# Performance work log

Measured on AMD Instinct MI355X. Metric: run time of the kernel, lower is better.

The kernel has to match this reference:

```python
import jax, jax.numpy as jnp
import numpy as np

B, S, H = 2, 2048, 2048
NH, NKV, HD = 16, 4, 128
ROPE_BASE = 10000.0


def setup_inputs() -> dict:
    key = jax.random.key(0)
    ks = jax.random.split(key, 5)
    x = jax.random.normal(ks[0], (B, S, H), dtype=jnp.float32)
    position_ids = jnp.arange(S, dtype=jnp.int64 if jax.config.jax_enable_x64 else jnp.int32).reshape(1, S)
    # Linear weights stored as [in, out] (equivalent to torch weight.T)
    sc = 1.0 / np.sqrt(H)
    Wq = jax.random.normal(ks[1], (H, NH * HD), dtype=jnp.float32) * sc
    Wk = jax.random.normal(ks[2], (H, NKV * HD), dtype=jnp.float32) * sc
    Wv = jax.random.normal(ks[3], (H, NKV * HD), dtype=jnp.float32) * sc
    Wo = jax.random.normal(ks[4], (NH * HD, H), dtype=jnp.float32) * (1.0 / np.sqrt(NH * HD))
    return {"x": x, "position_ids": position_ids, "Wq": Wq, "Wk": Wk, "Wv": Wv, "Wo": Wo}


def _rope(q, k, position_ids):
    # q: [B,S,NH,HD], k: [B,S,NKV,HD]; Llama-style half-split RoPE
    half = HD // 2
    inv_freq = 1.0 / (ROPE_BASE ** (jnp.arange(0, half, dtype=jnp.float32) * 2.0 / HD))
    ang = position_ids.astype(jnp.float32)[..., None] * inv_freq  # [b,S,half]
    cos = jnp.concatenate([jnp.cos(ang), jnp.cos(ang)], axis=-1)[:, :, None, :]  # [b,S,1,HD]
    sin = jnp.concatenate([jnp.sin(ang), jnp.sin(ang)], axis=-1)[:, :, None, :]

    def rot_half(t):
        t1, t2 = t[..., :half], t[..., half:]
        return jnp.concatenate([-t2, t1], axis=-1)

    return q * cos + rot_half(q) * sin, k * cos + rot_half(k) * sin


def reference(x, position_ids, Wq, Wk, Wv, Wo):
    b, s, _ = x.shape
    q = (x @ Wq).reshape(b, s, NH, HD)
    k = (x @ Wk).reshape(b, s, NKV, HD)
    v = (x @ Wv).reshape(b, s, NKV, HD)
    q, k = _rope(q, k, position_ids)
    reps = NH // NKV
    k = jnp.repeat(k, reps, axis=2)  # repeat_interleave on head dim
    v = jnp.repeat(v, reps, axis=2)
    q = q.transpose(0, 2, 1, 3)  # [b,h,s,d]
    k = k.transpose(0, 2, 1, 3)
    v = v.transpose(0, 2, 1, 3)
    scores = jnp.einsum('bhqd,bhkd->bhqk', q, k) / jnp.sqrt(jnp.float32(HD))
    causal = jnp.triu(jnp.ones((s, s), dtype=bool), k=1)
    scores = jnp.where(causal, -jnp.inf, scores)
    attn = jax.nn.softmax(scores.astype(jnp.float32), axis=-1).astype(q.dtype)
    out = jnp.einsum('bhqk,bhkd->bhqd', attn, v)
    out = out.transpose(0, 2, 1, 3).reshape(b, s, NH * HD)
    return out @ Wo
```

## Files before the change

### kernel.cpp

```cpp
#include <hip/hip_runtime.h>
#include <stdint.h>

typedef unsigned short u16;
typedef __attribute__((ext_vector_type(8))) short short8;
typedef __attribute__((ext_vector_type(4))) float floatx4;

#define S_LEN 2048
#define NQKV 3072

#if __has_builtin(__builtin_amdgcn_exp2f)
#define EXP2F __builtin_amdgcn_exp2f
#else
#define EXP2F exp2f
#endif

__device__ inline float bf2f(u16 u) {
  union { uint32_t u; float f; } v; v.u = ((uint32_t)u) << 16; return v.f;
}
__device__ inline u16 f2bf(float f) {
  union { float f; uint32_t u; } v; v.f = f;
  uint32_t r = v.u + 0x7fffu + ((v.u >> 16) & 1u);
  return (u16)(r >> 16);
}
__device__ inline void gl2lds16(const u16* g, u16* l) {
  __builtin_amdgcn_global_load_lds((const __attribute__((address_space(1))) uint32_t*)g,
                                   (__attribute__((address_space(3))) uint32_t*)l, 16, 0, 0);
}

__global__ void cast_k(const float* __restrict__ in, u16* __restrict__ out, int n4) {
  int i = blockIdx.x * 256 + threadIdx.x;
  if (i >= n4) return;
  float4 v = ((const float4*)in)[i];
  ushort4 o;
  o.x = f2bf(v.x); o.y = f2bf(v.y); o.z = f2bf(v.z); o.w = f2bf(v.w);
  ((ushort4*)out)[i] = o;
}

__global__ void transpose_k(const float* __restrict__ in, u16* __restrict__ out, int K, int N) {
  __shared__ u16 tile[32][33];
  int n0 = blockIdx.x * 32, k0 = blockIdx.y * 32;
  int tx = threadIdx.x, ty = threadIdx.y;
#pragma unroll
  for (int i = 0; i < 4; i++)
    tile[ty + 8 * i][tx] = f2bf(in[(size_t)(k0 + ty + 8 * i) * N + n0 + tx]);
  __syncthreads();
#pragma unroll
  for (int i = 0; i < 4; i++)
    out[(size_t)(n0 + ty + 8 * i) * K + k0 + tx] = tile[tx][ty + 8 * i];
}

__global__ void vtrans_k(const u16* __restrict__ qkv, u16* __restrict__ vt) {
  __shared__ u16 tile[32][33];
  int bk = blockIdx.x * 32, bd = blockIdx.y * 32, bz = blockIdx.z;
  int bb = bz >> 2, kvh = bz & 3;
  const u16* src = qkv + ((size_t)bb * S_LEN) * NQKV + 2560 + kvh * 128;
  u16* dst = vt + (size_t)bz * 128 * 2048;
  int tx = threadIdx.x, ty = threadIdx.y;
#pragma unroll
  for (int i = 0; i < 4; i++)
    tile[ty + 8 * i][tx] = src[(size_t)(bk + ty + 8 * i) * NQKV + bd + tx];
  __syncthreads();
#pragma unroll
  for (int i = 0; i < 4; i++)
    dst[(size_t)(bd + ty + 8 * i) * 2048 + bk + tx] = tile[tx][ty + 8 * i];
}

template <bool OUTF32>
__global__ __launch_bounds__(256) void gemm_bt(const u16* __restrict__ A, const u16* __restrict__ Bt,
                                               void* __restrict__ Cv, int M, int N, int K) {
  __shared__ u16 As[128 * 32];
  __shared__ u16 Bs[128 * 32];
  const int m0 = blockIdx.y * 128, n0 = blockIdx.x * 128;
  const int t = threadIdx.x, w = t >> 6, lane = t & 63;
  const int quad = lane >> 4, l16 = lane & 15;
  const int wm = (w >> 1) * 64, wn = (w & 1) * 64;
  const int lrow = lane >> 2, lk = (lane & 3) * 8;
  floatx4 acc[4][4] = {};
  for (int k0 = 0; k0 < K; k0 += 32) {
#pragma unroll
    for (int c = 2 * w; c <= 2 * w + 1; ++c) {
      int row = c * 16 + lrow;
      gl2lds16(A + (size_t)(m0 + row) * K + k0 + lk, As + c * 512 + lane * 8);
      gl2lds16(Bt + (size_t)(n0 + row) * K + k0 + lk, Bs + c * 512 + lane * 8);
    }
    __syncthreads();
    short8 a[4], b[4];
#pragma unroll
    for (int mt = 0; mt < 4; mt++) a[mt] = *(const short8*)(As + (wm + mt * 16 + l16) * 32 + quad * 8);
#pragma unroll
    for (int nt = 0; nt < 4; nt++) b[nt] = *(const short8*)(Bs + (wn + nt * 16 + l16) * 32 + quad * 8);
#pragma unroll
    for (int mt = 0; mt < 4; mt++)
#pragma unroll
      for (int nt = 0; nt < 4; nt++)
        acc[mt][nt] = __builtin_amdgcn_mfma_f32_16x16x32_bf16(a[mt], b[nt], acc[mt][nt], 0, 0, 0);
    __syncthreads();
  }
#pragma unroll
  for (int mt = 0; mt < 4; mt++)
#pragma unroll
    for (int nt = 0; nt < 4; nt++)
#pragma unroll
      for (int r = 0; r < 4; r++) {
        int row = m0 + wm + mt * 16 + quad * 4 + r;
        int col = n0 + wn + nt * 16 + l16;
        if (OUTF32)
          ((float*)Cv)[(size_t)row * N + col] = acc[mt][nt][r];
        else
          ((u16*)Cv)[(size_t)row * N + col] = f2bf(acc[mt][nt][r]);
      }
}

__global__ void rope_k(u16* __restrict__ qkv, const int* __restrict__ pos) {
  int idx = blockIdx.x * 256 + threadIdx.x;
  int i = idx & 63;
  int hh = (idx >> 6) % 20;
  int row = idx / (64 * 20);
  int s = row & (S_LEN - 1);
  float p = (float)pos[s];
  float freq = __expf(-(float)i * 0.015625f * 9.210340371976184f);
  float ang = p * freq;
  float c = cosf(ang), sn = sinf(ang);
  int col = (hh < 16) ? hh * 128 : 2048 + (hh - 16) * 128;
  size_t base = (size_t)row * NQKV + col + i;
  float t1 = bf2f(qkv[base]), t2 = bf2f(qkv[base + 64]);
  qkv[base] = f2bf(t1 * c - t2 * sn);
  qkv[base + 64] = f2bf(t2 * c + t1 * sn);
}

#define PL_LD 72
__global__ __launch_bounds__(256) void attn_k(const u16* __restrict__ qkv,
                                              const u16* __restrict__ vt,
                                              u16* __restrict__ ctx) {
  __shared__ u16 Kl[2][64 * 128];
  __shared__ u16 Vl[2][128 * 64];
  __shared__ u16 Pl[4][16 * PL_LD];
  const int p = blockIdx.x;
  const int h = blockIdx.y, bb = blockIdx.z;
  const int kvh = h >> 2;
  const int t = threadIdx.x, w = t >> 6, lane = t & 63;
  const int quad = lane >> 4, l16 = lane & 15;
  const int sx = l16 & 7;
  const int kkey0 = w * 16 + (lane >> 4);
  const int kslot = lane & 15;
  const int vd0 = w * 32 + (lane >> 3);
  const int vslot = lane & 7;
  const size_t rowbase = (size_t)bb * S_LEN;
  const u16* Kg0 = qkv + rowbase * NQKV + 2048 + kvh * 128;
  const u16* Vg0 = vt + (size_t)(bb * 4 + kvh) * 128 * 2048;
  const float c2 = 0.12751744f;
  short8 onesf = {16256, 16256, 16256, 16256, 16256, 16256, 16256, 16256};

  for (int phase = 0; phase < 2; phase++) {
    const int qt = phase ? p : 31 - p;
    const int rw = qt * 64 + w * 16;

    short8 qf[4];
#pragma unroll
    for (int ks = 0; ks < 4; ks++)
      qf[ks] = *(const short8*)(qkv + (rowbase + rw + l16) * NQKV + h * 128 + ks * 32 + quad * 8);

    floatx4 acc[8] = {};
    floatx4 accl = {0.f, 0.f, 0.f, 0.f};

    __syncthreads();
    {
      const u16* Kg = Kg0;
      const u16* Vg = Vg0;
#pragma unroll
      for (int ii = 0; ii < 4; ii++) {
        int key = kkey0 + ii * 4;
        gl2lds16(Kg + (size_t)key * NQKV + ((kslot ^ (key & 7)) * 8),
                 &Kl[0][0] + w * 2048 + ii * 512 + lane * 8);
      }
#pragma unroll
      for (int ii = 0; ii < 4; ii++) {
        int d = vd0 + ii * 8;
        gl2lds16(Vg + (size_t)d * 2048 + ((vslot ^ (d & 7)) * 8),
                 &Vl[0][0] + w * 2048 + ii * 512 + lane * 8);
      }
    }

    for (int kb = 0; kb <= qt; kb++) {
      const int cur = kb & 1;
      __syncthreads();
      if (kb < qt) {
        const u16* Kg = Kg0 + (size_t)(kb + 1) * 64 * NQKV;
        const u16* Vg = Vg0 + (kb + 1) * 64;
        u16* KlN = &Kl[cur ^ 1][0];
        u16* VlN = &Vl[cur ^ 1][0];
#pragma unroll
        for (int ii = 0; ii < 4; ii++) {
          int key = kkey0 + ii * 4;
          gl2lds16(Kg + (size_t)key * NQKV + ((kslot ^ (key & 7)) * 8),
                   KlN + w * 2048 + ii * 512 + lane * 8);
        }
#pragma unroll
        for (int ii = 0; ii < 4; ii++) {
          int d = vd0 + ii * 8;
          gl2lds16(Vg + (size_t)d * 2048 + ((vslot ^ (d & 7)) * 8),
                   VlN + w * 2048 + ii * 512 + lane * 8);
        }
      }
      const u16* KlB = &Kl[cur][0];
      const u16* VlB = &Vl[cur][0];

      floatx4 sc[4];
#pragma unroll
      for (int nt = 0; nt < 4; nt++) {
        const u16* Krow = KlB + (nt * 16 + l16) * 128;
        short8 kf[4];
#pragma unroll
        for (int ks = 0; ks < 4; ks++)
          kf[ks] = *(const short8*)(Krow + (((ks * 4 + quad) ^ sx) * 8));
        floatx4 s = {0.f, 0.f, 0.f, 0.f};
#pragma unroll
        for (int ks = 0; ks < 4; ks++) s = __builtin_amdgcn_mfma_f32_16x16x32_bf16(qf[ks], kf[ks], s, 0, 0, 0);
        sc[nt] = s;
      }
      const bool diag = (kb == qt);
#pragma unroll
      for (int nt = 0; nt < 4; nt++)
#pragma unroll
        for (int r = 0; r < 4; r++) {
          float e = EXP2F(sc[nt][r] * c2);
          if (diag) {
            int keyg = kb * 64 + nt * 16 + l16;
            int rowg = rw + quad * 4 + r;
            if (keyg > rowg) e = 0.f;
          }
          Pl[w][(quad * 4 + r) * PL_LD + nt * 16 + l16] = (u16)(__float_as_uint(e) >> 16);
        }
      short8 pf[2];
#pragma unroll
      for (int kh = 0; kh < 2; kh++)
        pf[kh] = *(const short8*)(&Pl[w][0] + l16 * PL_LD + kh * 32 + quad * 8);
      accl = __builtin_amdgcn_mfma_f32_16x16x32_bf16(pf[0], onesf, accl, 0, 0, 0);
      accl = __builtin_amdgcn_mfma_f32_16x16x32_bf16(pf[1], onesf, accl, 0, 0, 0);
#pragma unroll
      for (int nto = 0; nto < 8; nto++) {
        const u16* Vrow = VlB + (nto * 16 + l16) * 64;
        short8 vf0 = *(const short8*)(Vrow + ((quad ^ sx) * 8));
        short8 vf1 = *(const short8*)(Vrow + (((quad + 4) ^ sx) * 8));
        acc[nto] = __builtin_amdgcn_mfma_f32_16x16x32_bf16(pf[0], vf0, acc[nto], 0, 0, 0);
        acc[nto] = __builtin_amdgcn_mfma_f32_16x16x32_bf16(pf[1], vf1, acc[nto], 0, 0, 0);
      }
    }
#pragma unroll
    for (int r = 0; r < 4; r++) {
      float inv = 1.0f / accl[r];
      int rowg = rw + quad * 4 + r;
#pragma unroll
      for (int nto = 0; nto < 8; nto++) {
        int col = h * 128 + nto * 16 + l16;
        ctx[(rowbase + rowg) * 2048 + col] = f2bf(acc[nto][r] * inv);
      }
    }
  }
}

extern "C" void kernel_launch(void* const* d_in, const int* in_sizes, int n_in,
                              void* d_out, int out_size, void* d_ws, size_t ws_size,
                              hipStream_t stream) {
  const float* x  = (const float*)d_in[0];
  const int* pos  = (const int*)d_in[1];
  const float* Wq = (const float*)d_in[2];
  const float* Wk = (const float*)d_in[3];
  const float* Wv = (const float*)d_in[4];
  const float* Wo = (const float*)d_in[5];
  float* out = (float*)d_out;
  char* ws = (char*)d_ws;
  u16* Xb  = (u16*)(ws);
  u16* WT  = (u16*)(ws + 16777216);
  u16* WoT = (u16*)(ws + 29360128);
  u16* QKV = (u16*)(ws + 37748736);
  u16* CTX = (u16*)(ws + 62914560);
  u16* VT  = Xb;

  hipLaunchKernelGGL(cast_k, dim3(8192), dim3(256), 0, stream, x, Xb, 2097152);

  dim3 tb(32, 8);
  hipLaunchKernelGGL(transpose_k, dim3(64, 64), tb, 0, stream, Wq, WT, 2048, 2048);
  hipLaunchKernelGGL(transpose_k, dim3(16, 64), tb, 0, stream, Wk, WT + (size_t)2048 * 2048, 2048, 512);
  hipLaunchKernelGGL(transpose_k, dim3(16, 64), tb, 0, stream, Wv, WT + (size_t)2560 * 2048, 2048, 512);
  hipLaunchKernelGGL(transpose_k, dim3(64, 64), tb, 0, stream, Wo, WoT, 2048, 2048);

  hipLaunchKernelGGL(HIP_KERNEL_NAME(gemm_bt<false>), dim3(24, 32), dim3(256), 0, stream,
                     Xb, WT, (void*)QKV, 4096, 3072, 2048);
  hipLaunchKernelGGL(rope_k, dim3(20480), dim3(256), 0, stream, QKV, pos);
  hipLaunchKernelGGL(vtrans_k, dim3(64, 4, 8), tb, 0, stream, QKV, VT);
  hipLaunchKernelGGL(attn_k, dim3(16, 16, 2), dim3(256), 0, stream, QKV, VT, CTX);
  hipLaunchKernelGGL(HIP_KERNEL_NAME(gemm_bt<true>), dim3(16, 32), dim3(256), 0, stream,
                     CTX, WoT, (void*)out, 4096, 2048, 2048);
}
```

Measured before the change: 316.5 us.

## Replace QKV projection GEMM with 256x256-tile double-buffered 8-wave kernel

Adds a new bf16 GEMM kernel for the QKV projection that uses 256x256 output tiles, 512 threads, double-buffered LDS with an XOR swizzle, prefetch of the next K-tile split across four compute phases, s_setprio around the MFMA bursts, and an XCD-aware block remap. The larger tile raises data reuse per LDS load and overlaps global loads with MFMA work. In exchange it uses 128KB of LDS per block and a large accumulator register set, and launches only 192 blocks, which is below one wave of work on 256 CUs.

```diff
diff --git a/kernel.cpp b/kernel.cpp
--- a/kernel.cpp
+++ b/kernel.cpp
@@ -109,6 +109,110 @@
         else
           ((u16*)Cv)[(size_t)row * N + col] = f2bf(acc[mt][nt][r]);
       }
+}
+
+__global__ __launch_bounds__(512, 2) void gemm256_k(const u16* __restrict__ A,
+                                                    const u16* __restrict__ Bt,
+                                                    u16* __restrict__ C, int N, int K) {
+  __shared__ u16 Al[2][2][8192];
+  __shared__ u16 Bl[2][2][8192];
+  const int TN = N >> 8;
+  int flat = blockIdx.x;
+  const int cpx = gridDim.x >> 3;
+  flat = (flat & 7) * cpx + (flat >> 3);
+  const int m0 = (flat / TN) << 8, n0 = (flat % TN) << 8;
+  const int t = threadIdx.x, w = t >> 6, lane = t & 63;
+  const int quad = lane >> 4, l16 = lane & 15;
+  const int wm = w >> 2, wn = w & 3;
+  const int sr = t >> 3, sl = t & 7;
+  floatx4 acc[2][2][4][2] = {};
+  const int NKT = K >> 6;
+
+#pragma unroll
+  for (int round = 0; round < 2; round++) {
+    int r = round * 64 + sr;
+    int so = (sl ^ (r & 7)) << 3;
+    gl2lds16(A + (size_t)(m0 + r) * K + so, &Al[0][0][0] + round * 4096 + t * 8);
+    gl2lds16(Bt + (size_t)(n0 + r) * K + so, &Bl[0][0][0] + round * 4096 + t * 8);
+    gl2lds16(Bt + (size_t)(n0 + 128 + r) * K + so, &Bl[0][1][0] + round * 4096 + t * 8);
+    gl2lds16(A + (size_t)(m0 + 128 + r) * K + so, &Al[0][1][0] + round * 4096 + t * 8);
+  }
+  asm volatile("s_waitcnt vmcnt(0)" ::: "memory");
+  __builtin_amdgcn_s_barrier();
+
+  for (int kt = 0; kt < NKT; kt++) {
+    const int c = kt & 1;
+    const u16* Ab = &Al[c][0][0];
+    const u16* Bb = &Bl[c][0][0];
+    u16* An = &Al[c ^ 1][0][0];
+    u16* Bn = &Bl[c ^ 1][0][0];
+    const int k1 = (kt + 1) << 6;
+    const bool pf = (kt + 1 < NKT);
+#pragma unroll
+    for (int ph = 0; ph < 4; ph++) {
+      const int mh = ph >> 1, nh = ph & 1;
+      short8 af[4][2], bf[2][2];
+#pragma unroll
+      for (int mt = 0; mt < 4; mt++) {
+        int ra = wm * 64 + mt * 16 + l16;
+        const u16* base = Ab + mh * 8192 + ra * 64;
+#pragma unroll
+        for (int ks = 0; ks < 2; ks++)
+          af[mt][ks] = *(const short8*)(base + (((ks * 4 + quad) ^ (ra & 7)) << 3));
+      }
+#pragma unroll
+      for (int nt = 0; nt < 2; nt++) {
+        int rb = wn * 32 + nt * 16 + l16;
+        const u16* base = Bb + nh * 8192 + rb * 64;
+#pragma unroll
+        for (int ks = 0; ks < 2; ks++)
+          bf[nt][ks] = *(const short8*)(base + (((ks * 4 + quad) ^ (rb & 7)) << 3));
+      }
+      if (pf) {
+        const u16* G;
+        u16* L;
+        int rbase;
+        if (ph == 0)      { G = A;  L = An;        rbase = m0; }
+        else if (ph == 1) { G = Bt; L = Bn;        rbase = n0; }
+        else if (ph == 2) { G = Bt; L = Bn + 8192; rbase = n0 + 128; }
+        else              { G = A;  L = An + 8192; rbase = m0 + 128; }
+#pragma unroll
+        for (int round = 0; round < 2; round++) {
+          int r = round * 64 + sr;
+          gl2lds16(G + (size_t)(rbase + r) * K + k1 + ((sl ^ (r & 7)) << 3),
+                   L + round * 4096 + t * 8);
+        }
+      }
+      __builtin_amdgcn_s_barrier();
+      asm volatile("s_waitcnt lgkmcnt(0)" ::: "memory");
+      __builtin_amdgcn_s_setprio(1);
+#pragma unroll
+      for (int mt = 0; mt < 4; mt++)
+#pragma unroll
+        for (int nt = 0; nt < 2; nt++)
+#pragma unroll
+          for (int ks = 0; ks < 2; ks++)
+            acc[mh][nh][mt][nt] =
+                __builtin_amdgcn_mfma_f32_16x16x32_bf16(af[mt][ks], bf[nt][ks], acc[mh][nh][mt][nt], 0, 0, 0);
+      __builtin_amdgcn_s_setprio(0);
+      asm volatile("s_waitcnt vmcnt(4)" ::: "memory");
+      __builtin_amdgcn_s_barrier();
+    }
+  }
+#pragma unroll
+  for (int mh = 0; mh < 2; mh++)
+#pragma unroll
+    for (int nh = 0; nh < 2; nh++)
+#pragma unroll
+      for (int mt = 0; mt < 4; mt++)
+#pragma unroll
+        for (int nt = 0; nt < 2; nt++)
+#pragma unroll
+          for (int r = 0; r < 4; r++) {
+            int row = m0 + mh * 128 + wm * 64 + mt * 16 + quad * 4 + r;
+            int col = n0 + nh * 128 + wn * 32 + nt * 16 + l16;
+            C[(size_t)row * N + col] = f2bf(acc[mh][nh][mt][nt][r]);
+          }
 }
 
 __global__ void rope_k(u16* __restrict__ qkv, const int* __restrict__ pos) {
@@ -285,8 +389,7 @@
   hipLaunchKernelGGL(transpose_k, dim3(16, 64), tb, 0, stream, Wv, WT + (size_t)2560 * 2048, 2048, 512);
   hipLaunchKernelGGL(transpose_k, dim3(64, 64), tb, 0, stream, Wo, WoT, 2048, 2048);
 
-  hipLaunchKernelGGL(HIP_KERNEL_NAME(gemm_bt<false>), dim3(24, 32), dim3(256), 0, stream,
-                     Xb, WT, (void*)QKV, 4096, 3072, 2048);
+  hipLaunchKernelGGL(gemm256_k, dim3(192), dim3(512), 0, stream, Xb, WT, QKV, 3072, 2048);
   hipLaunchKernelGGL(rope_k, dim3(20480), dim3(256), 0, stream, QKV, pos);
   hipLaunchKernelGGL(vtrans_k, dim3(64, 4, 8), tb, 0, stream, QKV, VT);
   hipLaunchKernelGGL(attn_k, dim3(16, 16, 2), dim3(256), 0, stream, QKV, VT, CTX);
```

Measured after the change: 322.0 us. No clear change (+1.7%).
